# Kernel tuning notes

Hardware: AMD Instinct MI355X
Metric: run time of the kernel (lower is better)

Reference implementation:

```python
import jax, jax.numpy as jnp
import numpy as np

NUM_HEADS = 16

def setup_inputs() -> dict:
    key = jax.random.key(0)
    k1, k2, k3 = jax.random.split(key, 3)
    B, N, C = 4, 4096, 1024
    x = jax.random.normal(k1, (B, N, C), dtype=jnp.float32)
    y = jax.random.normal(k2, (B, N, C), dtype=jnp.float32)
    # nn.Linear(embed_dim, embed_dim): weight [C, C], bias [C]
    W_proj = jax.random.normal(k3, (C, C), dtype=jnp.float32) * (1.0 / np.sqrt(C))
    b_proj = jnp.zeros((C,), dtype=jnp.float32)
    return {"x": x, "y": y, "W_proj": W_proj, "b_proj": b_proj}

def reference(x, y, W_proj, b_proj):
    B, N, C = x.shape
    H = NUM_HEADS
    d = C // H
    # NOTE: no head transpose in the original -> scores are over the HEAD axis.
    q = x.reshape(B, N, H, d)
    k = y.reshape(B, N, H, d)
    v = y.reshape(B, N, H, d)
    # attn: [B, N, H, H], per-token head-to-head scores
    attn = jnp.einsum('bnhd,bngd->bnhg', q, k) / jnp.sqrt(jnp.asarray(d, x.dtype))
    attn = jax.nn.softmax(attn, axis=-1)
    # dropout(p=0.1) is identity in eval mode
    o = jnp.einsum('bnhg,bngd->bnhd', attn, v)          # [B, N, H, d]
    # x.transpose(1, 2).reshape(B, N, C) in torch:
    o = jnp.transpose(o, (0, 2, 1, 3)).reshape(B, N, C)
    out = o @ W_proj.T + b_proj
    return out
```

## Files before the change

### kernel.cpp

```cpp
#include <hip/hip_runtime.h>
#include <hip/hip_bf16.h>
#include <stdint.h>

typedef __attribute__((ext_vector_type(8))) short bf16x8;
typedef __attribute__((ext_vector_type(4))) short bf16x4;
typedef __attribute__((ext_vector_type(4))) float f32x4;
typedef __attribute__((ext_vector_type(4))) int   i32x4;

static __device__ __forceinline__ short f2bs(float f) {
  __hip_bfloat16 h = __float2bfloat16(f);
  return __builtin_bit_cast(short, h);
}

__device__ __forceinline__ void gload_lds16(const void* g, void* l) {
  auto* gp = reinterpret_cast<__attribute__((address_space(1))) uint32_t*>((uintptr_t)g);
  auto* lp = reinterpret_cast<__attribute__((address_space(3))) uint32_t*>((uintptr_t)l);
  __builtin_amdgcn_global_load_lds(gp, lp, 16, 0, 0);
}

__global__ __launch_bounds__(256) void attn_kernel(
    const float* __restrict__ x, const float* __restrict__ y,
    __hip_bfloat16* __restrict__ A,
    const float* __restrict__ W, __hip_bfloat16* __restrict__ Wb)
{
  if (blockIdx.x < 1024) {
    const int i = (blockIdx.x * 256 + threadIdx.x) * 4;
    const float4 v = *(const float4*)(W + i);
    Wb[i + 0] = __float2bfloat16(v.x);
    Wb[i + 1] = __float2bfloat16(v.y);
    Wb[i + 2] = __float2bfloat16(v.z);
    Wb[i + 3] = __float2bfloat16(v.w);
  }

  const int wid  = threadIdx.x >> 6;
  const int lane = threadIdx.x & 63;
  const int tok  = blockIdx.x * 4 + wid;
  const int b    = tok >> 12;
  const int n    = tok & 4095;

  const float* xr = x + (size_t)tok * 1024;
  const float* yr = y + (size_t)tok * 1024;

  const int c  = lane & 15;
  const int qq = lane >> 4;

  const int fbase = c * 64 + qq * 8;
  bf16x8 yf[2], xf[2];
  #pragma unroll
  for (int kk = 0; kk < 2; ++kk) {
    const float4 a0 = *(const float4*)(yr + fbase + kk * 32);
    const float4 a1 = *(const float4*)(yr + fbase + kk * 32 + 4);
    const float4 b0 = *(const float4*)(xr + fbase + kk * 32);
    const float4 b1 = *(const float4*)(xr + fbase + kk * 32 + 4);
    yf[kk] = bf16x8{f2bs(a0.x), f2bs(a0.y), f2bs(a0.z), f2bs(a0.w),
                    f2bs(a1.x), f2bs(a1.y), f2bs(a1.z), f2bs(a1.w)};
    xf[kk] = bf16x8{f2bs(b0.x), f2bs(b0.y), f2bs(b0.z), f2bs(b0.w),
                    f2bs(b1.x), f2bs(b1.y), f2bs(b1.z), f2bs(b1.w)};
  }

  f32x4 acc = {0.f, 0.f, 0.f, 0.f};
  acc = __builtin_amdgcn_mfma_f32_16x16x32_bf16(yf[0], xf[0], acc, 0, 0, 0);
  acc = __builtin_amdgcn_mfma_f32_16x16x32_bf16(yf[1], xf[1], acc, 0, 0, 0);

  float sc[4];
  #pragma unroll
  for (int r = 0; r < 4; ++r) sc[r] = acc[r] * 0.125f;
  float mx = fmaxf(fmaxf(sc[0], sc[1]), fmaxf(sc[2], sc[3]));
  mx = fmaxf(mx, __shfl_xor(mx, 16));
  mx = fmaxf(mx, __shfl_xor(mx, 32));
  float e[4];
  #pragma unroll
  for (int r = 0; r < 4; ++r) e[r] = __expf(sc[r] - mx);
  float sm = (e[0] + e[1]) + (e[2] + e[3]);
  sm += __shfl_xor(sm, 16);
  sm += __shfl_xor(sm, 32);
  const float inv = 1.0f / sm;
  float p[4];
  #pragma unroll
  for (int r = 0; r < 4; ++r) p[r] = e[r] * inv;

  f32x4 o[4];
  #pragma unroll
  for (int q = 0; q < 4; ++q) o[q] = f32x4{0.f, 0.f, 0.f, 0.f};

#if __has_builtin(__builtin_amdgcn_mfma_f32_16x16x16bf16_1k)
  const bf16x4 pa = {f2bs(p[0]), f2bs(p[1]), f2bs(p[2]), f2bs(p[3])};
  #pragma unroll
  for (int q = 0; q < 4; ++q) {
    bf16x4 bq;
    #pragma unroll
    for (int j = 0; j < 4; ++j)
      bq[j] = f2bs(yr[(qq * 4 + j) * 64 + q * 16 + c]);
    o[q] = __builtin_amdgcn_mfma_f32_16x16x16bf16_1k(pa, bq, o[q], 0, 0, 0);
  }
#else
  const int u0 = ((int)(unsigned short)f2bs(p[1]) << 16) | (unsigned short)f2bs(p[0]);
  const int u1 = ((int)(unsigned short)f2bs(p[3]) << 16) | (unsigned short)f2bs(p[2]);
  const int s0 = c + 32 * qq;
  int a0 = __shfl(u0, s0), a1 = __shfl(u1, s0);
  int a2 = __shfl(u0, s0 + 16), a3 = __shfl(u1, s0 + 16);
  const bool valid = (qq < 2);
  if (!valid) { a0 = 0; a1 = 0; a2 = 0; a3 = 0; }
  const bf16x8 a8 = __builtin_bit_cast(bf16x8, i32x4{a0, a1, a2, a3});
  #pragma unroll
  for (int q = 0; q < 4; ++q) {
    bf16x8 b8;
    #pragma unroll
    for (int j = 0; j < 8; ++j) {
      const int g = (qq * 8 + j) & 15;
      const float v = yr[g * 64 + q * 16 + c];
      b8[j] = valid ? f2bs(v) : (short)0;
    }
    o[q] = __builtin_amdgcn_mfma_f32_16x16x32_bf16(a8, b8, o[q], 0, 0, 0);
  }
#endif

  const size_t base = ((size_t)b * 4096 + (n >> 4)) * 1024 + ((n & 15) << 6) + c;
  #pragma unroll
  for (int q = 0; q < 4; ++q)
    #pragma unroll
    for (int r = 0; r < 4; ++r) {
      const int h = qq * 4 + r;
      A[base + (size_t)h * 262144 + q * 16] = __float2bfloat16(o[q][r]);
    }
}

__global__ __launch_bounds__(256, 3) void gemm_m97(
    const __hip_bfloat16* __restrict__ A,
    const __hip_bfloat16* __restrict__ Bw,
    const float* __restrict__ bias,
    float* __restrict__ C)
{
  __shared__ char ldsA[8192];
  __shared__ char ldsB[8192];

  const int tid  = threadIdx.x;
  const int lane = tid & 63;
  const int wid  = tid >> 6;
  const int wr   = wid >> 1;
  const int wcN  = wid & 1;

  const int bid = blockIdx.x;
  const int nb  = (bid & 7) * 128 + (bid >> 3);
  const int mBase = (nb >> 3) * 128;
  const int nBase = (nb & 7) * 128;

  const int srow = tid >> 2;
  const int lcb  = (((tid & 3) ^ ((srow >> 1) & 3)) << 4);
  const char* aS0 = (const char*)A  + (size_t)(mBase + srow)      * 2048 + lcb;
  const char* aS1 = (const char*)A  + (size_t)(mBase + 64 + srow) * 2048 + lcb;
  const char* bS0 = (const char*)Bw + (size_t)(nBase + srow)      * 2048 + lcb;
  const char* bS1 = (const char*)Bw + (size_t)(nBase + 64 + srow) * 2048 + lcb;
  char* aD = ldsA + tid * 16;
  char* bD = ldsB + tid * 16;

  const int fr = lane & 15;
  const int kq = lane >> 4;
  const int ofk  = ((kq ^ ((fr >> 1) & 3)) << 4);
  const int aOff = (wr  * 64 + fr) * 64 + ofk;
  const int bOff = (wcN * 64 + fr) * 64 + ofk;

  f32x4 acc[4][4];
  #pragma unroll
  for (int m = 0; m < 4; ++m)
    #pragma unroll
    for (int n = 0; n < 4; ++n) acc[m][n] = f32x4{0.f, 0.f, 0.f, 0.f};

  for (int ko = 0; ko < 2048; ko += 64) {
    gload_lds16(aS0 + ko, aD);
    gload_lds16(aS1 + ko, aD + 4096);
    gload_lds16(bS0 + ko, bD);
    gload_lds16(bS1 + ko, bD + 4096);
    __syncthreads();

    bf16x8 Af[4], Bf[4];
    #pragma unroll
    for (int n = 0; n < 4; ++n) Bf[n] = *(const bf16x8*)(ldsB + bOff + n * 1024);
    #pragma unroll
    for (int m = 0; m < 4; ++m) Af[m] = *(const bf16x8*)(ldsA + aOff + m * 1024);

    #pragma unroll
    for (int m = 0; m < 4; ++m)
      #pragma unroll
      for (int n = 0; n < 4; ++n)
        acc[m][n] = __builtin_amdgcn_mfma_f32_16x16x32_bf16(Af[m], Bf[n], acc[m][n], 0, 0, 0);
    __syncthreads();
  }

  #pragma unroll
  for (int n = 0; n < 4; ++n) {
    const int col = nBase + wcN * 64 + n * 16 + fr;
    const float bv = bias[col];
    #pragma unroll
    for (int m = 0; m < 4; ++m) {
      const int row0 = mBase + wr * 64 + m * 16 + kq * 4;
      #pragma unroll
      for (int r = 0; r < 4; ++r)
        C[(size_t)(row0 + r) * 1024 + col] = acc[m][n][r] + bv;
    }
  }
}

extern "C" void kernel_launch(void* const* d_in, const int* in_sizes, int n_in,
                              void* d_out, int out_size, void* d_ws, size_t ws_size,
                              hipStream_t stream) {
  const float* x    = (const float*)d_in[0];
  const float* y    = (const float*)d_in[1];
  const float* W    = (const float*)d_in[2];
  const float* bias = (const float*)d_in[3];
  float* out = (float*)d_out;

  __hip_bfloat16* Abuf = (__hip_bfloat16*)d_ws;
  __hip_bfloat16* Wbuf = (__hip_bfloat16*)((char*)d_ws + (size_t)16384 * 1024 * 2);

  attn_kernel<<<4096, 256, 0, stream>>>(x, y, Abuf, W, Wbuf);
  gemm_m97<<<1024, 256, 0, stream>>>(Abuf, Wbuf, bias, out);
}
```

Measured before the change: 76.73 us.

## Pre-tile A and W into MFMA fragment layout and load GEMM operands directly

The attention kernel and the weight conversion now write their bf16 outputs in a blocked layout that matches the MFMA fragment order. This lets the GEMM load operands straight from global memory into registers, with no LDS staging and no __syncthreads. The GEMM double-buffers fragments in registers, prefetching two k-steps ahead, and raises wave priority with s_setprio around the MFMA bursts. In exchange it relies on L2/L1 for reuse across waves, since each wave now fetches its own fragments instead of sharing a block-wide LDS tile, and it needs more registers.

```diff
diff --git a/kernel.cpp b/kernel.cpp
--- a/kernel.cpp
+++ b/kernel.cpp
@@ -12,11 +12,6 @@
   return __builtin_bit_cast(short, h);
 }
 
-__device__ __forceinline__ void gload_lds16(const void* g, void* l) {
-  auto* gp = reinterpret_cast<__attribute__((address_space(1))) uint32_t*>((uintptr_t)g);
-  auto* lp = reinterpret_cast<__attribute__((address_space(3))) uint32_t*>((uintptr_t)l);
-  __builtin_amdgcn_global_load_lds(gp, lp, 16, 0, 0);
-}
 
 __global__ __launch_bounds__(256) void attn_kernel(
     const float* __restrict__ x, const float* __restrict__ y,
@@ -26,10 +21,13 @@
   if (blockIdx.x < 1024) {
     const int i = (blockIdx.x * 256 + threadIdx.x) * 4;
     const float4 v = *(const float4*)(W + i);
-    Wb[i + 0] = __float2bfloat16(v.x);
-    Wb[i + 1] = __float2bfloat16(v.y);
-    Wb[i + 2] = __float2bfloat16(v.z);
-    Wb[i + 3] = __float2bfloat16(v.w);
+    const int nW = i >> 10, kW = i & 1023;
+    const size_t o = (size_t)(nW >> 7) * 131072 + (size_t)(kW >> 5) * 4096
+                   + (size_t)((nW >> 4) & 7) * 512 + (nW & 15) * 32 + (kW & 31);
+    Wb[o + 0] = __float2bfloat16(v.x);
+    Wb[o + 1] = __float2bfloat16(v.y);
+    Wb[o + 2] = __float2bfloat16(v.z);
+    Wb[o + 3] = __float2bfloat16(v.w);
   }
 
   const int wid  = threadIdx.x >> 6;
@@ -115,25 +113,29 @@
   }
 #endif
 
-  const size_t base = ((size_t)b * 4096 + (n >> 4)) * 1024 + ((n & 15) << 6) + c;
+  const int n16 = n >> 4;
+  const size_t base2 = (size_t)(b * 32 + (n16 >> 7)) * 131072
+                     + (size_t)((n & 15) * 2) * 4096
+                     + (size_t)((n16 >> 4) & 7) * 512 + (n16 & 15) * 32 + c;
   #pragma unroll
   for (int q = 0; q < 4; ++q)
     #pragma unroll
     for (int r = 0; r < 4; ++r) {
       const int h = qq * 4 + r;
-      A[base + (size_t)h * 262144 + q * 16] = __float2bfloat16(o[q][r]);
-    }
-}
-
-__global__ __launch_bounds__(256, 3) void gemm_m97(
+      A[base2 + (size_t)h * 262144 + (q >> 1) * 4096 + (q & 1) * 16] =
+          __float2bfloat16(o[q][r]);
+    }
+}
+
+#define SP1   __builtin_amdgcn_s_setprio(1)
+#define SP0   __builtin_amdgcn_s_setprio(0)
+
+__global__ __launch_bounds__(256, 3) void gemm_direct(
     const __hip_bfloat16* __restrict__ A,
     const __hip_bfloat16* __restrict__ Bw,
     const float* __restrict__ bias,
     float* __restrict__ C)
 {
-  __shared__ char ldsA[8192];
-  __shared__ char ldsB[8192];
-
   const int tid  = threadIdx.x;
   const int lane = tid & 63;
   const int wid  = tid >> 6;
@@ -142,23 +144,16 @@
 
   const int bid = blockIdx.x;
   const int nb  = (bid & 7) * 128 + (bid >> 3);
-  const int mBase = (nb >> 3) * 128;
-  const int nBase = (nb & 7) * 128;
-
-  const int srow = tid >> 2;
-  const int lcb  = (((tid & 3) ^ ((srow >> 1) & 3)) << 4);
-  const char* aS0 = (const char*)A  + (size_t)(mBase + srow)      * 2048 + lcb;
-  const char* aS1 = (const char*)A  + (size_t)(mBase + 64 + srow) * 2048 + lcb;
-  const char* bS0 = (const char*)Bw + (size_t)(nBase + srow)      * 2048 + lcb;
-  const char* bS1 = (const char*)Bw + (size_t)(nBase + 64 + srow) * 2048 + lcb;
-  char* aD = ldsA + tid * 16;
-  char* bD = ldsB + tid * 16;
+  const int mt  = nb >> 3;
+  const int nt  = nb & 7;
 
   const int fr = lane & 15;
   const int kq = lane >> 4;
-  const int ofk  = ((kq ^ ((fr >> 1) & 3)) << 4);
-  const int aOff = (wr  * 64 + fr) * 64 + ofk;
-  const int bOff = (wcN * 64 + fr) * 64 + ofk;
+
+  const __hip_bfloat16* aP = A  + (size_t)mt * 131072 + (wr  * 4) * 512
+                           + fr * 32 + kq * 8;
+  const __hip_bfloat16* bP = Bw + (size_t)nt * 131072 + (wcN * 4) * 512
+                           + fr * 32 + kq * 8;
 
   f32x4 acc[4][4];
   #pragma unroll
@@ -166,34 +161,56 @@
     #pragma unroll
     for (int n = 0; n < 4; ++n) acc[m][n] = f32x4{0.f, 0.f, 0.f, 0.f};
 
-  for (int ko = 0; ko < 2048; ko += 64) {
-    gload_lds16(aS0 + ko, aD);
-    gload_lds16(aS1 + ko, aD + 4096);
-    gload_lds16(bS0 + ko, bD);
-    gload_lds16(bS1 + ko, bD + 4096);
-    __syncthreads();
-
-    bf16x8 Af[4], Bf[4];
-    #pragma unroll
-    for (int n = 0; n < 4; ++n) Bf[n] = *(const bf16x8*)(ldsB + bOff + n * 1024);
-    #pragma unroll
-    for (int m = 0; m < 4; ++m) Af[m] = *(const bf16x8*)(ldsA + aOff + m * 1024);
-
+  bf16x8 A0[4], B0[4], A1[4], B1[4];
+
+  #pragma unroll
+  for (int f = 0; f < 4; ++f) {
+    A0[f] = *(const bf16x8*)(aP + f * 512);
+    B0[f] = *(const bf16x8*)(bP + f * 512);
+  }
+  #pragma unroll
+  for (int f = 0; f < 4; ++f) {
+    A1[f] = *(const bf16x8*)(aP + 4096 + f * 512);
+    B1[f] = *(const bf16x8*)(bP + 4096 + f * 512);
+  }
+
+  #pragma unroll 2
+  for (int ks = 0; ks < 32; ks += 2) {
+    const int k2 = (ks + 2) & 31;
+    const int k3 = (ks + 3) & 31;
+    SP1;
     #pragma unroll
     for (int m = 0; m < 4; ++m)
       #pragma unroll
       for (int n = 0; n < 4; ++n)
-        acc[m][n] = __builtin_amdgcn_mfma_f32_16x16x32_bf16(Af[m], Bf[n], acc[m][n], 0, 0, 0);
-    __syncthreads();
+        acc[m][n] = __builtin_amdgcn_mfma_f32_16x16x32_bf16(A0[m], B0[n], acc[m][n], 0, 0, 0);
+    SP0;
+    #pragma unroll
+    for (int f = 0; f < 4; ++f) {
+      A0[f] = *(const bf16x8*)(aP + k2 * 4096 + f * 512);
+      B0[f] = *(const bf16x8*)(bP + k2 * 4096 + f * 512);
+    }
+    SP1;
+    #pragma unroll
+    for (int m = 0; m < 4; ++m)
+      #pragma unroll
+      for (int n = 0; n < 4; ++n)
+        acc[m][n] = __builtin_amdgcn_mfma_f32_16x16x32_bf16(A1[m], B1[n], acc[m][n], 0, 0, 0);
+    SP0;
+    #pragma unroll
+    for (int f = 0; f < 4; ++f) {
+      A1[f] = *(const bf16x8*)(aP + k3 * 4096 + f * 512);
+      B1[f] = *(const bf16x8*)(bP + k3 * 4096 + f * 512);
+    }
   }
 
   #pragma unroll
   for (int n = 0; n < 4; ++n) {
-    const int col = nBase + wcN * 64 + n * 16 + fr;
+    const int col = nt * 128 + wcN * 64 + n * 16 + fr;
     const float bv = bias[col];
     #pragma unroll
     for (int m = 0; m < 4; ++m) {
-      const int row0 = mBase + wr * 64 + m * 16 + kq * 4;
+      const int row0 = mt * 128 + wr * 64 + m * 16 + kq * 4;
       #pragma unroll
       for (int r = 0; r < 4; ++r)
         C[(size_t)(row0 + r) * 1024 + col] = acc[m][n][r] + bv;
@@ -214,5 +231,5 @@
   __hip_bfloat16* Wbuf = (__hip_bfloat16*)((char*)d_ws + (size_t)16384 * 1024 * 2);
 
   attn_kernel<<<4096, 256, 0, stream>>>(x, y, Abuf, W, Wbuf);
-  gemm_m97<<<1024, 256, 0, stream>>>(Abuf, Wbuf, bias, out);
-}
+  gemm_direct<<<1024, 256, 0, stream>>>(Abuf, Wbuf, bias, out);
+}
```

New measurement: 100.1 us. 30.4% more time.

## Pipeline GEMM with 4-stage LDS ring buffer and 512-thread blocks

Applied to the files above, without the earlier changes.

Replaces the single-buffered GEMM loop with a 4-slot LDS ring. Async global-to-LDS loads for stage k+3 are issued while stage k is being computed, and explicit vmcnt waits gate each stage. The block grows to 512 threads (8 waves, 2x4 layout), each wave computing a 64x32 sub-tile, and s_setprio raises priority around the MFMA bursts. The aim is to hide global memory latency behind matrix work and drop one barrier per iteration. In exchange it uses 64KB of LDS per block, which lowers the number of resident blocks, and each wave reuses fewer fragments.

```diff
diff --git a/kernel.cpp b/kernel.cpp
--- a/kernel.cpp
+++ b/kernel.cpp
@@ -125,20 +125,28 @@
     }
 }
 
-__global__ __launch_bounds__(256, 3) void gemm_m97(
+#define FENCE asm volatile("" ::: "memory")
+#define BAR   __builtin_amdgcn_s_barrier()
+#define VM4   asm volatile("s_waitcnt vmcnt(4)" ::: "memory")
+#define VM2   asm volatile("s_waitcnt vmcnt(2)" ::: "memory")
+#define VM0   asm volatile("s_waitcnt vmcnt(0)" ::: "memory")
+#define SP1   __builtin_amdgcn_s_setprio(1)
+#define SP0   __builtin_amdgcn_s_setprio(0)
+
+__global__ __launch_bounds__(512, 2) void gemm_r4(
     const __hip_bfloat16* __restrict__ A,
     const __hip_bfloat16* __restrict__ Bw,
     const float* __restrict__ bias,
     float* __restrict__ C)
 {
-  __shared__ char ldsA[8192];
-  __shared__ char ldsB[8192];
+  __shared__ char ldsA[4 * 8192];
+  __shared__ char ldsB[4 * 8192];
 
   const int tid  = threadIdx.x;
   const int lane = tid & 63;
   const int wid  = tid >> 6;
-  const int wr   = wid >> 1;
-  const int wcN  = wid & 1;
+  const int wr   = wid >> 2;
+  const int wc   = wid & 3;
 
   const int bid = blockIdx.x;
   const int nb  = (bid & 7) * 128 + (bid >> 3);
@@ -146,50 +154,66 @@
   const int nBase = (nb & 7) * 128;
 
   const int srow = tid >> 2;
-  const int lcb  = (((tid & 3) ^ ((srow >> 1) & 3)) << 4);
-  const char* aS0 = (const char*)A  + (size_t)(mBase + srow)      * 2048 + lcb;
-  const char* aS1 = (const char*)A  + (size_t)(mBase + 64 + srow) * 2048 + lcb;
-  const char* bS0 = (const char*)Bw + (size_t)(nBase + srow)      * 2048 + lcb;
-  const char* bS1 = (const char*)Bw + (size_t)(nBase + 64 + srow) * 2048 + lcb;
+  const int lcb  = (((tid & 3) ^ ((tid >> 3) & 3)) << 4);
+  const char* aS = (const char*)A  + (size_t)(mBase + srow) * 2048 + lcb;
+  const char* bS = (const char*)Bw + (size_t)(nBase + srow) * 2048 + lcb;
   char* aD = ldsA + tid * 16;
   char* bD = ldsB + tid * 16;
 
   const int fr = lane & 15;
   const int kq = lane >> 4;
   const int ofk  = ((kq ^ ((fr >> 1) & 3)) << 4);
-  const int aOff = (wr  * 64 + fr) * 64 + ofk;
-  const int bOff = (wcN * 64 + fr) * 64 + ofk;
-
-  f32x4 acc[4][4];
+  const int aOff = (wr * 64 + fr) * 64 + ofk;
+  const int bOff = (wc * 32 + fr) * 64 + ofk;
+
+  f32x4 acc[4][2];
   #pragma unroll
   for (int m = 0; m < 4; ++m)
     #pragma unroll
-    for (int n = 0; n < 4; ++n) acc[m][n] = f32x4{0.f, 0.f, 0.f, 0.f};
-
-  for (int ko = 0; ko < 2048; ko += 64) {
-    gload_lds16(aS0 + ko, aD);
-    gload_lds16(aS1 + ko, aD + 4096);
-    gload_lds16(bS0 + ko, bD);
-    gload_lds16(bS1 + ko, bD + 4096);
-    __syncthreads();
-
-    bf16x8 Af[4], Bf[4];
-    #pragma unroll
-    for (int n = 0; n < 4; ++n) Bf[n] = *(const bf16x8*)(ldsB + bOff + n * 1024);
-    #pragma unroll
-    for (int m = 0; m < 4; ++m) Af[m] = *(const bf16x8*)(ldsA + aOff + m * 1024);
-
+    for (int n = 0; n < 2; ++n) acc[m][n] = f32x4{0.f, 0.f, 0.f, 0.f};
+
+  auto STG = [&](int sp) {
+    gload_lds16(aS + sp * 64, aD + ((sp & 3) << 13));
+    gload_lds16(bS + sp * 64, bD + ((sp & 3) << 13));
+  };
+
+  auto BODY = [&](int s, int gate, bool stg) {
+    if (gate == 4) { VM4; } else if (gate == 2) { VM2; } else { VM0; }
+    FENCE; BAR; FENCE;
+    if (stg) STG(s + 3);
+    const char* aB = ldsA + ((s & 3) << 13) + aOff;
+    const char* bB = ldsB + ((s & 3) << 13) + bOff;
+    bf16x8 Af[4], Bf[2];
+    #pragma unroll
+    for (int n = 0; n < 2; ++n) Bf[n] = *(const bf16x8*)(bB + n * 1024);
+    #pragma unroll
+    for (int m = 0; m < 4; ++m) Af[m] = *(const bf16x8*)(aB + m * 1024);
+    SP1;
     #pragma unroll
     for (int m = 0; m < 4; ++m)
       #pragma unroll
-      for (int n = 0; n < 4; ++n)
+      for (int n = 0; n < 2; ++n)
         acc[m][n] = __builtin_amdgcn_mfma_f32_16x16x32_bf16(Af[m], Bf[n], acc[m][n], 0, 0, 0);
-    __syncthreads();
-  }
-
-  #pragma unroll
-  for (int n = 0; n < 4; ++n) {
-    const int col = nBase + wcN * 64 + n * 16 + fr;
+    SP0;
+  };
+
+  STG(0); STG(1); STG(2);
+
+  for (int g = 0; g < 7; ++g) {
+    const int s = g * 4;
+    BODY(s + 0, 4, true);
+    BODY(s + 1, 4, true);
+    BODY(s + 2, 4, true);
+    BODY(s + 3, 4, true);
+  }
+  BODY(28, 4, true);
+  BODY(29, 4, false);
+  BODY(30, 2, false);
+  BODY(31, 0, false);
+
+  #pragma unroll
+  for (int n = 0; n < 2; ++n) {
+    const int col = nBase + wc * 32 + n * 16 + fr;
     const float bv = bias[col];
     #pragma unroll
     for (int m = 0; m < 4; ++m) {
@@ -214,5 +238,5 @@
   __hip_bfloat16* Wbuf = (__hip_bfloat16*)((char*)d_ws + (size_t)16384 * 1024 * 2);
 
   attn_kernel<<<4096, 256, 0, stream>>>(x, y, Abuf, W, Wbuf);
-  gemm_m97<<<1024, 256, 0, stream>>>(Abuf, Wbuf, bias, out);
-}
+  gemm_r4<<<1024, 512, 0, stream>>>(Abuf, Wbuf, bias, out);
+}
```

Result: no change. 75.39 us (-1.7%).
